# Kernel optimization log

Measured on AMD Instinct MI355X. Metric: run time of the kernel, lower is better.

Reference implementation:

```python
import jax, jax.numpy as jnp
import numpy as np

T, N, E, D_IN, D_OUT = 8, 50000, 800000, 64, 64


def setup_inputs() -> dict:
    key = jax.random.key(0)
    k = jax.random.split(key, 7)
    x = jax.random.normal(k[0], (T, N, D_IN), dtype=jnp.float32)
    edge_index = jax.random.randint(k[1], (2, E), 0, N, dtype=jnp.int32)
    edge_time = jax.random.uniform(k[2], (E,), dtype=jnp.float32)
    node_time = jnp.sort(jax.random.uniform(k[3], (T,), dtype=jnp.float32))
    edge_weight = jax.random.uniform(k[4], (E,), dtype=jnp.float32)
    W = jax.random.normal(k[5], (D_IN, D_OUT), dtype=jnp.float32) / jnp.sqrt(jnp.float32(D_IN))
    b = jnp.zeros((D_OUT,), dtype=jnp.float32)
    return {"x": x, "edge_index": edge_index, "edge_time": edge_time,
            "node_time": node_time, "edge_weight": edge_weight, "W": W, "b": b}


def reference(x, edge_index, edge_time, node_time, edge_weight, W, b):
    # Faithful translation of DGN.forward: per-timestep temporal GNN conv.
    # DGNConv (assumed canonical form): edges with edge_time <= node_time[i]
    # are active; messages x[src]*edge_weight are sum-scattered to dst, then a
    # Linear(in, out) is applied. lax.scan replaces the Python time loop.
    src, dst = edge_index[0], edge_index[1]

    def step(_, xt_t):
        xt, t = xt_t  # xt: [N, D_IN], t: scalar
        w = jnp.where(edge_time <= t, edge_weight, jnp.float32(0.0))  # [E]
        msg = xt[src] * w[:, None]                                    # [E, D_IN]
        agg = jax.ops.segment_sum(msg, dst, num_segments=N)           # [N, D_IN]
        return None, agg @ W + b                                      # [N, D_OUT]

    _, out = jax.lax.scan(step, None, (x, node_time))
    return out  # [T, N, D_OUT]
```

## Files before the change

kernel.cpp:

```cpp
#include <hip/hip_runtime.h>
#include <cstdint>
#include <cstddef>

#define TSTEPS 8
#define D 64

static __device__ __forceinline__ unsigned short f2bf(float f) {
    unsigned int u = __float_as_uint(f);
    return (unsigned short)((u + 0x7FFFu + ((u >> 16) & 1u)) >> 16);
}
static __device__ __forceinline__ float bf2f(unsigned short h) {
    return __uint_as_float(((unsigned int)h) << 16);
}

__global__ __launch_bounds__(256) void prep_kernel(
    const float* __restrict__ x, unsigned short* __restrict__ xb,
    const int* __restrict__ dst, const float* __restrict__ etime,
    const float* __restrict__ ntime,
    int* __restrict__ cnt, unsigned short* __restrict__ rankA,
    int E, int N, int histBlocks, int blocksPerPlane)
{
    int tid = threadIdx.x;
    if ((int)blockIdx.x < histBlocks) {
        int e = blockIdx.x * 256 + tid;
        if (e < E) {
            float et = etime[e];
            int t0 = 0;
#pragma unroll
            for (int t = 0; t < TSTEPS; t++) t0 += (ntime[t] < et) ? 1 : 0;
            if (t0 < TSTEPS)
                rankA[e] = (unsigned short)atomicAdd(&cnt[dst[e]], 1);
        }
    } else {
        int bb = blockIdx.x - histBlocks;
        int t  = bb / blocksPerPlane;
        int r  = bb - t * blocksPerPlane;
        int j  = r * 256 + tid;
        int d4 = j & 15;
        int n  = j >> 4;
        if (n < N) {
            float4 v = ((const float4*)x)[((size_t)t * N + n) * 16 + d4];
            ushort4 u;
            u.x = f2bf(v.x); u.y = f2bf(v.y); u.z = f2bf(v.z); u.w = f2bf(v.w);
            ((ushort4*)xb)[(size_t)n * 128 + t * 16 + d4] = u;
        }
    }
}

__global__ __launch_bounds__(256) void reduce_kernel(const int* __restrict__ cnt,
                                                     int* __restrict__ sums, int n) {
    __shared__ int red[256];
    int tid = threadIdx.x;
    int base = blockIdx.x * 1024 + tid * 4;
    int tot = 0;
#pragma unroll
    for (int j = 0; j < 4; j++) { int i = base + j; tot += (i < n) ? cnt[i] : 0; }
    red[tid] = tot;
    __syncthreads();
    for (int s = 128; s > 0; s >>= 1) {
        if (tid < s) red[tid] += red[tid + s];
        __syncthreads();
    }
    if (tid == 0) sums[blockIdx.x] = red[0];
}

__global__ __launch_bounds__(256) void scanwrite_kernel(const int* __restrict__ cnt,
                                                        const int* __restrict__ sums,
                                                        int* __restrict__ rowptr, int n) {
    __shared__ int buf[256];
    int tid = threadIdx.x;
    int base = blockIdx.x * 1024 + tid * 4;
    int v[4];
    int tot = 0;
#pragma unroll
    for (int j = 0; j < 4; j++) { int i = base + j; v[j] = (i < n) ? cnt[i] : 0; tot += v[j]; }

    buf[tid] = tot;
    __syncthreads();
    for (int off = 1; off < 256; off <<= 1) {
        int t = (tid >= off) ? buf[tid - off] : 0;
        __syncthreads();
        buf[tid] += t;
        __syncthreads();
    }
    int exclThread = buf[tid] - tot;

    int bp = 0;
    for (int j = 0; j < blockIdx.x; j++) bp += sums[j];

    int running = bp + exclThread;
#pragma unroll
    for (int j = 0; j < 4; j++) {
        int i = base + j;
        if (i < n) { rowptr[i] = running; running += v[j]; }
    }
    if (blockIdx.x == (int)gridDim.x - 1 && tid == 255) rowptr[n] = running;
}

__global__ __launch_bounds__(256) void bucket_kernel(
    const int* __restrict__ src, const int* __restrict__ dst,
    const float* __restrict__ etime, const float* __restrict__ ew,
    const float* __restrict__ ntime, int E,
    const unsigned short* __restrict__ rankA, const int* __restrict__ rowptr,
    uint2* __restrict__ meta)
{
    int e = blockIdx.x * 256 + threadIdx.x;
    if (e >= E) return;
    float et = etime[e];
    int t0 = 0;
#pragma unroll
    for (int t = 0; t < TSTEPS; t++) t0 += (ntime[t] < et) ? 1 : 0;
    if (t0 >= TSTEPS) return;
    int p = rowptr[dst[e]] + (int)rankA[e];
    uint2 m;
    m.x = ((unsigned int)src[e] << 3) | (unsigned int)t0;
    m.y = __float_as_uint(ew[e]);
    meta[p] = m;
}

template<bool USE_BF16>
__global__ __launch_bounds__(256) void fused_gather_kernel(
    const float* __restrict__ xf, const unsigned short* __restrict__ xb,
    const uint2* __restrict__ meta, const int* __restrict__ rowptr,
    const float* __restrict__ W, const float* __restrict__ b,
    float* __restrict__ out, int N)
{
    __shared__ float Wlds[64 * 64];
    __shared__ float aggS[4][TSTEPS][64];

    int tid = threadIdx.x;
#pragma unroll
    for (int i = 0; i < 16; i++) Wlds[tid + i * 256] = W[tid + i * 256];
    __syncthreads();

    int wslot = tid >> 6;
    int lane  = tid & 63;
    int g = lane >> 4;
    int q = lane & 15;
    int n = blockIdx.x * 4 + wslot;

    const size_t plane = (size_t)N * D;

    float4 acc[TSTEPS];
#pragma unroll
    for (int t = 0; t < TSTEPS; t++) acc[t] = make_float4(0.f, 0.f, 0.f, 0.f);

    if (n < N) {
        int p0 = rowptr[n], p1 = rowptr[n + 1];
        for (int p = p0; p < p1; p += 8) {
            int i0 = p + g, i1 = p + g + 4;
            if (USE_BF16) {
                if (i0 < p1) {
                    uint2 m = meta[i0];
                    int t0 = (int)(m.x & 7u);
                    float w = __uint_as_float(m.y);
                    const unsigned short* xp = xb + ((size_t)(m.x >> 3) << 9) + (q << 2);
#pragma unroll
                    for (int t = 0; t < TSTEPS; t++) {
                        if (t >= t0) {
                            ushort4 u = *reinterpret_cast<const ushort4*>(xp + (t << 6));
                            acc[t].x = fmaf(bf2f(u.x), w, acc[t].x);
                            acc[t].y = fmaf(bf2f(u.y), w, acc[t].y);
                            acc[t].z = fmaf(bf2f(u.z), w, acc[t].z);
                            acc[t].w = fmaf(bf2f(u.w), w, acc[t].w);
                        }
                    }
                }
                if (i1 < p1) {
                    uint2 m = meta[i1];
                    int t0 = (int)(m.x & 7u);
                    float w = __uint_as_float(m.y);
                    const unsigned short* xp = xb + ((size_t)(m.x >> 3) << 9) + (q << 2);
#pragma unroll
                    for (int t = 0; t < TSTEPS; t++) {
                        if (t >= t0) {
                            ushort4 u = *reinterpret_cast<const ushort4*>(xp + (t << 6));
                            acc[t].x = fmaf(bf2f(u.x), w, acc[t].x);
                            acc[t].y = fmaf(bf2f(u.y), w, acc[t].y);
                            acc[t].z = fmaf(bf2f(u.z), w, acc[t].z);
                            acc[t].w = fmaf(bf2f(u.w), w, acc[t].w);
                        }
                    }
                }
            } else {
                if (i0 < p1) {
                    uint2 m = meta[i0];
                    int t0 = (int)(m.x & 7u);
                    float w = __uint_as_float(m.y);
                    const float4* xp = reinterpret_cast<const float4*>(
                        xf + (size_t)(m.x >> 3) * D) + q;
#pragma unroll
                    for (int t = 0; t < TSTEPS; t++) {
                        if (t >= t0) {
                            float4 v = xp[(size_t)t * (plane >> 2)];
                            acc[t].x = fmaf(v.x, w, acc[t].x);
                            acc[t].y = fmaf(v.y, w, acc[t].y);
                            acc[t].z = fmaf(v.z, w, acc[t].z);
                            acc[t].w = fmaf(v.w, w, acc[t].w);
                        }
                    }
                }
                if (i1 < p1) {
                    uint2 m = meta[i1];
                    int t0 = (int)(m.x & 7u);
                    float w = __uint_as_float(m.y);
                    const float4* xp = reinterpret_cast<const float4*>(
                        xf + (size_t)(m.x >> 3) * D) + q;
#pragma unroll
                    for (int t = 0; t < TSTEPS; t++) {
                        if (t >= t0) {
                            float4 v = xp[(size_t)t * (plane >> 2)];
                            acc[t].x = fmaf(v.x, w, acc[t].x);
                            acc[t].y = fmaf(v.y, w, acc[t].y);
                            acc[t].z = fmaf(v.z, w, acc[t].z);
                            acc[t].w = fmaf(v.w, w, acc[t].w);
                        }
                    }
                }
            }
        }
    }

#pragma unroll
    for (int t = 0; t < TSTEPS; t++) {
        acc[t].x += __shfl_xor(acc[t].x, 16); acc[t].y += __shfl_xor(acc[t].y, 16);
        acc[t].z += __shfl_xor(acc[t].z, 16); acc[t].w += __shfl_xor(acc[t].w, 16);
        acc[t].x += __shfl_xor(acc[t].x, 32); acc[t].y += __shfl_xor(acc[t].y, 32);
        acc[t].z += __shfl_xor(acc[t].z, 32); acc[t].w += __shfl_xor(acc[t].w, 32);
    }

    if (lane < 16) {
#pragma unroll
        for (int t = 0; t < TSTEPS; t++)
            *reinterpret_cast<float4*>(&aggS[wslot][t][lane * 4]) = acc[t];
    }
    __syncthreads();

    float o[TSTEPS];
    float bias = b[lane];
#pragma unroll
    for (int t = 0; t < TSTEPS; t++) o[t] = bias;

    for (int kc = 0; kc < 16; kc++) {
        float w0 = Wlds[(4 * kc + 0) * 64 + lane];
        float w1 = Wlds[(4 * kc + 1) * 64 + lane];
        float w2 = Wlds[(4 * kc + 2) * 64 + lane];
        float w3 = Wlds[(4 * kc + 3) * 64 + lane];
#pragma unroll
        for (int t = 0; t < TSTEPS; t++) {
            float4 a = *reinterpret_cast<const float4*>(&aggS[wslot][t][4 * kc]);
            o[t] = fmaf(a.x, w0, fmaf(a.y, w1, fmaf(a.z, w2, fmaf(a.w, w3, o[t]))));
        }
    }

    if (n < N) {
        size_t ob = (size_t)n * D + lane;
#pragma unroll
        for (int t = 0; t < TSTEPS; t++) out[(size_t)t * plane + ob] = o[t];
    }
}

extern "C" void kernel_launch(void* const* d_in, const int* in_sizes, int n_in,
                              void* d_out, int out_size, void* d_ws, size_t ws_size,
                              hipStream_t stream)
{
    const float* x     = (const float*)d_in[0];
    const int*   eidx  = (const int*)d_in[1];
    const float* etime = (const float*)d_in[2];
    const float* ntime = (const float*)d_in[3];
    const float* ew    = (const float*)d_in[4];
    const float* W     = (const float*)d_in[5];
    const float* b     = (const float*)d_in[6];
    float* out = (float*)d_out;

    const int T = in_sizes[3];
    const int E = in_sizes[1] / 2;
    const int N = in_sizes[0] / (T * D);

    const int* src = eidx;
    const int* dst = eidx + E;

    int nb = (N + 1023) / 1024;

    char* base = (char*)d_ws;
    uint2* meta   = (uint2*)base;
    int*   cnt    = (int*)(base + 8ll * E);
    int*   rowptr = cnt + N;
    int*   sums   = rowptr + N + 1;
    unsigned short* rankA = (unsigned short*)(sums + nb);
    size_t offX = 8ll * E + 4ll * (2ll * N + 1 + nb) + 2ll * E;
    offX = (offX + 15) & ~(size_t)15;
    unsigned short* xb = (unsigned short*)(base + offX);
    size_t needB = offX + 2ll * (size_t)T * N * D;
    bool useBf16 = (ws_size >= needB);

    hipMemsetAsync(cnt, 0, (size_t)N * sizeof(int), stream);

    int histBlocks = (E + 255) / 256;
    int blocksPerPlane = (16 * N + 255) / 256;
    int prepGrid = useBf16 ? (histBlocks + T * blocksPerPlane) : histBlocks;

    prep_kernel<<<prepGrid, 256, 0, stream>>>(x, xb, dst, etime, ntime,
                                              cnt, rankA, E, N, histBlocks,
                                              blocksPerPlane);
    reduce_kernel<<<nb, 256, 0, stream>>>(cnt, sums, N);
    scanwrite_kernel<<<nb, 256, 0, stream>>>(cnt, sums, rowptr, N);
    bucket_kernel<<<histBlocks, 256, 0, stream>>>(src, dst, etime, ew, ntime, E,
                                                  rankA, rowptr, meta);

    if (useBf16) {
        fused_gather_kernel<true><<<(N + 3) / 4, 256, 0, stream>>>(
            x, xb, meta, rowptr, W, b, out, N);
    } else {
        fused_gather_kernel<false><<<(N + 3) / 4, 256, 0, stream>>>(
            x, xb, meta, rowptr, W, b, out, N);
    }
}
```

Before: 466.9 us.

## Bucket edges by (dst, start timestep) and read W from global memory

The counting sort now keys edges on dst*8+t0 instead of dst alone, so each node's edge list comes out ordered by first active timestep. This should make the per-timestep `t >= t0` branches in the gather more uniform across a wave. The 16 KB shared-memory copy of W is dropped in favour of cached global reads, and launch bounds are raised to target higher occupancy. The prefix scan now runs in place over an 8x larger count array, which adds scan work: each block serially sums more partial sums.

```diff
diff --git a/kernel.cpp b/kernel.cpp
--- a/kernel.cpp
+++ b/kernel.cpp
@@ -28,8 +28,10 @@
             int t0 = 0;
 #pragma unroll
             for (int t = 0; t < TSTEPS; t++) t0 += (ntime[t] < et) ? 1 : 0;
-            if (t0 < TSTEPS)
-                rankA[e] = (unsigned short)atomicAdd(&cnt[dst[e]], 1);
+            if (t0 < TSTEPS) {
+                int key = dst[e] * 8 + t0;
+                rankA[e] = (unsigned short)atomicAdd(&cnt[key], 1);
+            }
         }
     } else {
         int bb = blockIdx.x - histBlocks;
@@ -64,9 +66,9 @@
     if (tid == 0) sums[blockIdx.x] = red[0];
 }
 
-__global__ __launch_bounds__(256) void scanwrite_kernel(const int* __restrict__ cnt,
+__global__ __launch_bounds__(256) void scanwrite_kernel(int* __restrict__ cnt,
                                                         const int* __restrict__ sums,
-                                                        int* __restrict__ rowptr, int n) {
+                                                        int n) {
     __shared__ int buf[256];
     int tid = threadIdx.x;
     int base = blockIdx.x * 1024 + tid * 4;
@@ -92,9 +94,9 @@
 #pragma unroll
     for (int j = 0; j < 4; j++) {
         int i = base + j;
-        if (i < n) { rowptr[i] = running; running += v[j]; }
-    }
-    if (blockIdx.x == (int)gridDim.x - 1 && tid == 255) rowptr[n] = running;
+        if (i < n) { cnt[i] = running; running += v[j]; }
+    }
+    if (blockIdx.x == (int)gridDim.x - 1 && tid == 255) cnt[n] = running;
 }
 
 __global__ __launch_bounds__(256) void bucket_kernel(
@@ -111,28 +113,24 @@
 #pragma unroll
     for (int t = 0; t < TSTEPS; t++) t0 += (ntime[t] < et) ? 1 : 0;
     if (t0 >= TSTEPS) return;
-    int p = rowptr[dst[e]] + (int)rankA[e];
+    int s = src[e];
+    int p = rowptr[dst[e] * 8 + t0] + (int)rankA[e];
     uint2 m;
-    m.x = ((unsigned int)src[e] << 3) | (unsigned int)t0;
+    m.x = ((unsigned int)s << 3) | (unsigned int)t0;
     m.y = __float_as_uint(ew[e]);
     meta[p] = m;
 }
 
 template<bool USE_BF16>
-__global__ __launch_bounds__(256) void fused_gather_kernel(
+__global__ __launch_bounds__(256, 8) void fused_gather_kernel(
     const float* __restrict__ xf, const unsigned short* __restrict__ xb,
     const uint2* __restrict__ meta, const int* __restrict__ rowptr,
     const float* __restrict__ W, const float* __restrict__ b,
     float* __restrict__ out, int N)
 {
-    __shared__ float Wlds[64 * 64];
     __shared__ float aggS[4][TSTEPS][64];
 
     int tid = threadIdx.x;
-#pragma unroll
-    for (int i = 0; i < 16; i++) Wlds[tid + i * 256] = W[tid + i * 256];
-    __syncthreads();
-
     int wslot = tid >> 6;
     int lane  = tid & 63;
     int g = lane >> 4;
@@ -146,7 +144,7 @@
     for (int t = 0; t < TSTEPS; t++) acc[t] = make_float4(0.f, 0.f, 0.f, 0.f);
 
     if (n < N) {
-        int p0 = rowptr[n], p1 = rowptr[n + 1];
+        int p0 = rowptr[8 * n], p1 = rowptr[8 * n + 8];
         for (int p = p0; p < p1; p += 8) {
             int i0 = p + g, i1 = p + g + 4;
             if (USE_BF16) {
@@ -241,11 +239,12 @@
 #pragma unroll
     for (int t = 0; t < TSTEPS; t++) o[t] = bias;
 
+    const float* Wc = W + lane;
     for (int kc = 0; kc < 16; kc++) {
-        float w0 = Wlds[(4 * kc + 0) * 64 + lane];
-        float w1 = Wlds[(4 * kc + 1) * 64 + lane];
-        float w2 = Wlds[(4 * kc + 2) * 64 + lane];
-        float w3 = Wlds[(4 * kc + 3) * 64 + lane];
+        float w0 = Wc[(4 * kc + 0) * 64];
+        float w1 = Wc[(4 * kc + 1) * 64];
+        float w2 = Wc[(4 * kc + 2) * 64];
+        float w3 = Wc[(4 * kc + 3) * 64];
 #pragma unroll
         for (int t = 0; t < TSTEPS; t++) {
             float4 a = *reinterpret_cast<const float4*>(&aggS[wslot][t][4 * kc]);
@@ -276,25 +275,25 @@
     const int T = in_sizes[3];
     const int E = in_sizes[1] / 2;
     const int N = in_sizes[0] / (T * D);
+    const int N8 = N * 8;
 
     const int* src = eidx;
     const int* dst = eidx + E;
 
-    int nb = (N + 1023) / 1024;
+    int nb = (N8 + 1023) / 1024;
 
     char* base = (char*)d_ws;
     uint2* meta   = (uint2*)base;
     int*   cnt    = (int*)(base + 8ll * E);
-    int*   rowptr = cnt + N;
-    int*   sums   = rowptr + N + 1;
+    int*   sums   = cnt + N8 + 1;
     unsigned short* rankA = (unsigned short*)(sums + nb);
-    size_t offX = 8ll * E + 4ll * (2ll * N + 1 + nb) + 2ll * E;
+    size_t offX = 8ll * E + 4ll * ((size_t)N8 + 1 + nb) + 2ll * E;
     offX = (offX + 15) & ~(size_t)15;
     unsigned short* xb = (unsigned short*)(base + offX);
     size_t needB = offX + 2ll * (size_t)T * N * D;
     bool useBf16 = (ws_size >= needB);
 
-    hipMemsetAsync(cnt, 0, (size_t)N * sizeof(int), stream);
+    hipMemsetAsync(cnt, 0, ((size_t)N8 + 1) * sizeof(int), stream);
 
     int histBlocks = (E + 255) / 256;
     int blocksPerPlane = (16 * N + 255) / 256;
@@ -303,16 +302,16 @@
     prep_kernel<<<prepGrid, 256, 0, stream>>>(x, xb, dst, etime, ntime,
                                               cnt, rankA, E, N, histBlocks,
                                               blocksPerPlane);
-    reduce_kernel<<<nb, 256, 0, stream>>>(cnt, sums, N);
-    scanwrite_kernel<<<nb, 256, 0, stream>>>(cnt, sums, rowptr, N);
+    reduce_kernel<<<nb, 256, 0, stream>>>(cnt, sums, N8);
+    scanwrite_kernel<<<nb, 256, 0, stream>>>(cnt, sums, N8);
     bucket_kernel<<<histBlocks, 256, 0, stream>>>(src, dst, etime, ew, ntime, E,
-                                                  rankA, rowptr, meta);
+                                                  rankA, cnt, meta);
 
     if (useBf16) {
         fused_gather_kernel<true><<<(N + 3) / 4, 256, 0, stream>>>(
-            x, xb, meta, rowptr, W, b, out, N);
+            x, xb, meta, cnt, W, b, out, N);
     } else {
         fused_gather_kernel<false><<<(N + 3) / 4, 256, 0, stream>>>(
-            x, xb, meta, rowptr, W, b, out, N);
-    }
-}
+            x, xb, meta, cnt, W, b, out, N);
+    }
+}
```

Measured after the change: 486.2 us. 1.04x slower.
